# Performance work log

Hardware: AMD Instinct MI355X
Metric: run time of the kernel (lower is better)

## Reference

```python
import jax, jax.numpy as jnp
import numpy as np

N_NODES = 100000
N_EDGES = 1600000

def setup_inputs() -> dict:
    key = jax.random.key(0)
    ks = jax.random.split(key, 6)
    x = jax.random.normal(ks[0], (N_NODES, 128), dtype=jnp.float32)
    edge_index = jax.random.randint(ks[1], (2, N_EDGES), 0, N_NODES, dtype=jnp.int64)
    edge_weight = jax.random.uniform(ks[2], (N_EDGES,), dtype=jnp.float32)
    # kaiming-uniform-like init for weights, zeros for biases (as in reset_parameters)
    bound1 = float(np.sqrt(6.0 / 128))
    W1 = jax.random.uniform(ks[3], (128, 128), minval=-bound1, maxval=bound1, dtype=jnp.float32)
    b1 = jnp.zeros((128,), dtype=jnp.float32)
    W2 = jax.random.uniform(ks[4], (128, 64), minval=-bound1, maxval=bound1, dtype=jnp.float32)
    b2 = jnp.zeros((64,), dtype=jnp.float32)
    return {"x": x, "edge_index": edge_index, "edge_weight": edge_weight,
            "W1": W1, "b1": b1, "W2": W2, "b2": b2}

def _gcn_conv(x, src, dst, ew, W, b):
    support = x @ W                      # [N, F_out] dense GEMM
    msgs = ew[:, None] * support[src]    # [E, F_out] gather + scale (spmm values)
    out = jax.ops.segment_sum(msgs, dst, num_segments=N_NODES)  # scatter-add
    return out + b

def reference(x, edge_index, edge_weight, W1, b1, W2, b2):
    dst, src = edge_index[0], edge_index[1]  # adj[dst, src] = edge_weight
    h = _gcn_conv(x, src, dst, edge_weight, W1, b1)
    h = jax.nn.relu(h)
    out = _gcn_conv(h, src, dst, edge_weight, W2, b2)
    return out
```

## Files before the change

kernel.cpp:

```cpp
#include <hip/hip_runtime.h>

#define N_NODES 100000
#define N_EDGES 1600000
#define NB 391
#define PAD 16
#define SC_EPB 2048
#define SC_BLOCKS ((N_EDGES + SC_EPB - 1) / SC_EPB)
#define LDA 136
#define NTILES ((N_NODES + 127) / 128)

typedef unsigned int uint32;
typedef __attribute__((ext_vector_type(8))) short bf16x8;
typedef __attribute__((ext_vector_type(4))) float f32x4;

__device__ __forceinline__ uint32 bf16_rne(float f) {
    uint32 u = __float_as_uint(f);
    return (u + 0x7fffu + ((u >> 16) & 1u)) >> 16;
}
__device__ __forceinline__ uint32 pack_bf16x2(float lo, float hi) {
    return bf16_rne(lo) | (bf16_rne(hi) << 16);
}
__device__ __forceinline__ float bf16_lo(uint32 u) { return __uint_as_float(u << 16); }
__device__ __forceinline__ float bf16_hi(uint32 u) { return __uint_as_float(u & 0xFFFF0000u); }

__global__ __launch_bounds__(256) void conv_x(const float* __restrict__ x,
                                              uint32* __restrict__ xb) {
    const int t = blockIdx.x * 256 + threadIdx.x;
    if (t >= N_NODES * 64) return;
    const float2 v = ((const float2*)x)[t];
    xb[t] = pack_bf16x2(v.x, v.y);
}

__global__ __launch_bounds__(256) void conv_w(const float* __restrict__ W1,
                                              const float* __restrict__ W2,
                                              uint32* __restrict__ w1tb,
                                              uint32* __restrict__ w2tb) {
    const int t = blockIdx.x * 256 + threadIdx.x;
    if (t < 128 * 64) {
        const int n = t >> 6, kk = t & 63;
        w1tb[t] = pack_bf16x2(W1[(2 * kk) * 128 + n], W1[(2 * kk + 1) * 128 + n]);
    } else if (t < 128 * 64 + 64 * 64) {
        const int u = t - 128 * 64;
        const int n = u >> 6, kk = u & 63;
        w2tb[u] = pack_bf16x2(W2[(2 * kk) * 64 + n], W2[(2 * kk + 1) * 64 + n]);
    }
}

__global__ __launch_bounds__(256) void bucket_hist(const int* __restrict__ dst,
                                                   int* __restrict__ bktCnt) {
    __shared__ int h[NB];
    for (int i = threadIdx.x; i < NB; i += 256) h[i] = 0;
    __syncthreads();
    for (int e = blockIdx.x * 256 + threadIdx.x; e < N_EDGES; e += NB * 256)
        atomicAdd(&h[dst[e] >> 8], 1);
    __syncthreads();
    for (int i = threadIdx.x; i < NB; i += 256)
        if (h[i]) atomicAdd(&bktCnt[i * PAD], h[i]);
}

__global__ __launch_bounds__(512) void bucket_scan(const int* __restrict__ bktCnt,
                                                   int* __restrict__ bBase,
                                                   int* __restrict__ bCur,
                                                   int* __restrict__ offs) {
    __shared__ int s[512];
    const int t = threadIdx.x;
    int v = (t < NB) ? bktCnt[t * PAD] : 0;
    s[t] = v;
    __syncthreads();
#pragma unroll
    for (int off = 1; off < 512; off <<= 1) {
        int u = (t >= off) ? s[t - off] : 0;
        __syncthreads();
        s[t] += u;
        __syncthreads();
    }
    if (t < NB) {
        const int excl = s[t] - v;
        bBase[t] = excl;
        bCur[t * PAD] = excl;
    }
    if (t == 0) {
        bBase[NB] = N_EDGES;
        offs[N_NODES] = N_EDGES;
    }
}

__global__ __launch_bounds__(256) void bucket_scatter2(const int* __restrict__ dst,
                                                       const int* __restrict__ src,
                                                       const float* __restrict__ ew,
                                                       int* __restrict__ bCur,
                                                       int2* __restrict__ bucketed) {
    __shared__ int h[NB];
    __shared__ int cur[NB];
    const int base = blockIdx.x * SC_EPB;
    const int end  = min(base + SC_EPB, N_EDGES);

    for (int i = threadIdx.x; i < NB; i += 256) h[i] = 0;
    __syncthreads();
    for (int e = base + threadIdx.x; e < end; e += 256)
        atomicAdd(&h[dst[e] >> 8], 1);
    __syncthreads();
    for (int i = threadIdx.x; i < NB; i += 256) {
        const int c = h[i];
        cur[i] = c ? atomicAdd(&bCur[i * PAD], c) : 0;
    }
    __syncthreads();
    for (int e = base + threadIdx.x; e < end; e += 256) {
        const int d = dst[e];
        const int p = atomicAdd(&cur[d >> 8], 1);
        bucketed[p] = make_int2(src[e] | ((d & 255) << 17), __float_as_int(ew[e]));
    }
}

__global__ __launch_bounds__(256) void bucket_csr(const int2* __restrict__ bucketed,
                                                  const int* __restrict__ bBase,
                                                  int* __restrict__ offs,
                                                  int2* __restrict__ csr_ef) {
    __shared__ int sdeg[256];
    __shared__ int lcur[256];
    const int b   = blockIdx.x;
    const int t   = threadIdx.x;
    const int beg = bBase[b], end = bBase[b + 1];

    sdeg[t] = 0;
    __syncthreads();
    for (int j = beg + t; j < end; j += 256)
        atomicAdd(&sdeg[(bucketed[j].x >> 17) & 255], 1);
    __syncthreads();
    const int mydeg = sdeg[t];
#pragma unroll
    for (int off = 1; off < 256; off <<= 1) {
        int u = (t >= off) ? sdeg[t - off] : 0;
        __syncthreads();
        sdeg[t] += u;
        __syncthreads();
    }
    const int excl = sdeg[t] - mydeg;
    lcur[t] = excl;
    const int node = b * 256 + t;
    if (node < N_NODES) offs[node] = beg + excl;
    __syncthreads();

    for (int j = beg + t; j < end; j += 256) {
        const int2 v = bucketed[j];
        const int dl = (v.x >> 17) & 255;
        const int p  = beg + atomicAdd(&lcur[dl], 1);
        csr_ef[p] = make_int2(v.x & 0x1FFFF, v.y);
    }
}

template <int FEAT>
__global__ __launch_bounds__(256) void aggregate(const void* __restrict__ featv,
                                                 const int* __restrict__ offs,
                                                 const int2* __restrict__ csr_ef,
                                                 const float* __restrict__ bias,
                                                 void* __restrict__ outv) {
    const int n    = (blockIdx.x * 256 + threadIdx.x) >> 6;
    const int lane = threadIdx.x & 63;
    if (n >= N_NODES) return;
    const int beg = offs[n], end = offs[n + 1];

    if constexpr (FEAT == 128) {
        const uint32* feat = (const uint32*)featv;
        float2 acc = make_float2(0.f, 0.f);
        int j = beg;
        for (; j + 3 < end; j += 4) {
            const int2 e0 = csr_ef[j],     e1 = csr_ef[j + 1];
            const int2 e2 = csr_ef[j + 2], e3 = csr_ef[j + 3];
            const uint32 v0 = feat[(size_t)e0.x * 64 + lane];
            const uint32 v1 = feat[(size_t)e1.x * 64 + lane];
            const uint32 v2 = feat[(size_t)e2.x * 64 + lane];
            const uint32 v3 = feat[(size_t)e3.x * 64 + lane];
            const float w0 = __int_as_float(e0.y), w1 = __int_as_float(e1.y);
            const float w2 = __int_as_float(e2.y), w3 = __int_as_float(e3.y);
            acc.x += w0 * bf16_lo(v0) + w1 * bf16_lo(v1) + w2 * bf16_lo(v2) + w3 * bf16_lo(v3);
            acc.y += w0 * bf16_hi(v0) + w1 * bf16_hi(v1) + w2 * bf16_hi(v2) + w3 * bf16_hi(v3);
        }
        for (; j < end; ++j) {
            const int2 e0 = csr_ef[j];
            const uint32 v = feat[(size_t)e0.x * 64 + lane];
            const float w = __int_as_float(e0.y);
            acc.x += w * bf16_lo(v);
            acc.y += w * bf16_hi(v);
        }
        ((uint32*)outv)[(size_t)n * 64 + lane] = pack_bf16x2(acc.x, acc.y);
    } else {
        const unsigned short* feat = (const unsigned short*)featv;
        float acc = bias[lane];
        int j = beg;
        for (; j + 3 < end; j += 4) {
            const int2 e0 = csr_ef[j],     e1 = csr_ef[j + 1];
            const int2 e2 = csr_ef[j + 2], e3 = csr_ef[j + 3];
            const float f0 = __uint_as_float((uint32)feat[(size_t)e0.x * 64 + lane] << 16);
            const float f1 = __uint_as_float((uint32)feat[(size_t)e1.x * 64 + lane] << 16);
            const float f2 = __uint_as_float((uint32)feat[(size_t)e2.x * 64 + lane] << 16);
            const float f3 = __uint_as_float((uint32)feat[(size_t)e3.x * 64 + lane] << 16);
            acc += __int_as_float(e0.y) * f0 + __int_as_float(e1.y) * f1
                 + __int_as_float(e2.y) * f2 + __int_as_float(e3.y) * f3;
        }
        for (; j < end; ++j) {
            const int2 e0 = csr_ef[j];
            acc += __int_as_float(e0.y)
                 * __uint_as_float((uint32)feat[(size_t)e0.x * 64 + lane] << 16);
        }
        ((float*)outv)[(size_t)n * 64 + lane] = acc;
    }
}

__global__ __launch_bounds__(512) void gemm_fused(const uint32* __restrict__ aggPb,
                                                  const uint32* __restrict__ w1tb,
                                                  const float* __restrict__ b1,
                                                  const uint32* __restrict__ w2tb,
                                                  uint32* __restrict__ sup2b, int N) {
    __shared__ __align__(16) short As[128 * LDA];
    __shared__ __align__(16) short W1s[128 * LDA];
    __shared__ __align__(16) short W2s[64 * LDA];
    __shared__ __align__(16) short Ts[128 * LDA];

    const int tid = threadIdx.x;

    for (int i = tid; i < 128 * 16; i += 512)
        *(uint4*)&W1s[(i >> 4) * LDA + (i & 15) * 8] = ((const uint4*)w1tb)[i];
    for (int i = tid; i < 64 * 16; i += 512)
        *(uint4*)&W2s[(i >> 4) * LDA + (i & 15) * 8] = ((const uint4*)w2tb)[i];

    const int wave = tid >> 6;
    const int lane = tid & 63;
    const int m    = lane & 15;
    const int quad = lane >> 4;
    const int rowbase = (wave & 3) * 32;
    const int colbase = (wave >> 2) * 64;

    float b1r[4];
#pragma unroll
    for (int ct = 0; ct < 4; ++ct) b1r[ct] = b1[colbase + ct * 16 + m];

    for (int tile = blockIdx.x; tile < NTILES; tile += gridDim.x) {
        const int row0 = tile * 128;
        __syncthreads();

#pragma unroll
        for (int i = 0; i < 4; ++i) {
            const int idx = i * 512 + tid;
            const int row = idx >> 4, c4 = idx & 15;
            const int grow = row0 + row;
            uint4 v = make_uint4(0u, 0u, 0u, 0u);
            if (grow < N) v = ((const uint4*)aggPb)[(size_t)grow * 16 + c4];
            *(uint4*)&As[row * LDA + c4 * 8] = v;
        }
        __syncthreads();

        bf16x8 afrag[2][4];
#pragma unroll
        for (int ss = 0; ss < 2; ++ss)
#pragma unroll
            for (int ch = 0; ch < 4; ++ch)
                afrag[ss][ch] = *(const bf16x8*)&As[(rowbase + ss * 16 + m) * LDA + ch * 32 + quad * 8];

        f32x4 acc[2][4];
#pragma unroll
        for (int ss = 0; ss < 2; ++ss)
#pragma unroll
            for (int ct = 0; ct < 4; ++ct) acc[ss][ct] = (f32x4){0.f, 0.f, 0.f, 0.f};

#pragma unroll
        for (int ct = 0; ct < 4; ++ct) {
            bf16x8 bfr[4];
#pragma unroll
            for (int ch = 0; ch < 4; ++ch)
                bfr[ch] = *(const bf16x8*)&W1s[(colbase + ct * 16 + m) * LDA + ch * 32 + quad * 8];
#pragma unroll
            for (int ss = 0; ss < 2; ++ss)
#pragma unroll
                for (int ch = 0; ch < 4; ++ch)
                    acc[ss][ct] = __builtin_amdgcn_mfma_f32_16x16x32_bf16(
                        afrag[ss][ch], bfr[ch], acc[ss][ct], 0, 0, 0);
        }

#pragma unroll
        for (int ss = 0; ss < 2; ++ss)
#pragma unroll
            for (int ct = 0; ct < 4; ++ct)
#pragma unroll
                for (int r = 0; r < 4; ++r) {
                    const float v = fmaxf(acc[ss][ct][r] + b1r[ct], 0.f);
                    const int row = rowbase + ss * 16 + quad * 4 + r;
                    const int col = colbase + ct * 16 + m;
                    Ts[row * LDA + col] = (short)bf16_rne(v);
                }
        __syncthreads();

        const int rb2 = wave * 16;
        bf16x8 tfrag[4];
#pragma unroll
        for (int ch = 0; ch < 4; ++ch)
            tfrag[ch] = *(const bf16x8*)&Ts[(rb2 + m) * LDA + ch * 32 + quad * 8];

        f32x4 acc2[4];
#pragma unroll
        for (int ct = 0; ct < 4; ++ct) acc2[ct] = (f32x4){0.f, 0.f, 0.f, 0.f};
#pragma unroll
        for (int ct = 0; ct < 4; ++ct)
#pragma unroll
            for (int ch = 0; ch < 4; ++ch) {
                const bf16x8 bfr = *(const bf16x8*)&W2s[(ct * 16 + m) * LDA + ch * 32 + quad * 8];
                acc2[ct] = __builtin_amdgcn_mfma_f32_16x16x32_bf16(
                    tfrag[ch], bfr, acc2[ct], 0, 0, 0);
            }

#pragma unroll
        for (int ct = 0; ct < 4; ++ct)
#pragma unroll
            for (int r = 0; r < 4; ++r) {
                const int row = rb2 + quad * 4 + r;
                const int col = ct * 16 + m;
                As[row * LDA + col] = (short)bf16_rne(acc2[ct][r]);
            }
        __syncthreads();
#pragma unroll
        for (int i = 0; i < 2; ++i) {
            const int idx = i * 512 + tid;
            const int row = idx >> 3, c4 = idx & 7;
            if (row0 + row < N)
                ((uint4*)sup2b)[(size_t)(row0 + row) * 8 + c4] = *(uint4*)&As[row * LDA + c4 * 8];
        }
    }
}

extern "C" void kernel_launch(void* const* d_in, const int* in_sizes, int n_in,
                              void* d_out, int out_size, void* d_ws, size_t ws_size,
                              hipStream_t stream) {
    const float* x  = (const float*)d_in[0];
    const int*   ei = (const int*)d_in[1];
    const float* ew = (const float*)d_in[2];
    const float* W1 = (const float*)d_in[3];
    const float* b1 = (const float*)d_in[4];
    const float* W2 = (const float*)d_in[5];
    const float* b2 = (const float*)d_in[6];
    float* out = (float*)d_out;

    const int* dstIdx = ei;
    const int* srcIdx = ei + N_EDGES;

    uint32* xb      = (uint32*)d_ws;
    uint32* aggPb   = xb + (size_t)N_NODES * 64;
    uint32* w1tb    = aggPb + (size_t)N_NODES * 64;
    uint32* w2tb    = w1tb + 128 * 64;
    int2*   csr_ef  = (int2*)(xb + (size_t)N_NODES * 64 + (size_t)N_NODES * 128);
    int*    bktCnt  = (int*)(csr_ef + N_EDGES);
    int*    bCur    = bktCnt + NB * PAD;
    int*    bBase   = bCur + NB * PAD;
    int*    offs    = bBase + NB + 1;
    int2*   bucketed = (int2*)aggPb;
    uint32* sup2b   = xb;

    (void)hipMemsetAsync(bktCnt, 0, (size_t)NB * PAD * sizeof(int), stream);
    conv_x<<<(N_NODES * 64 + 255) / 256, 256, 0, stream>>>(x, xb);
    conv_w<<<48, 256, 0, stream>>>(W1, W2, w1tb, w2tb);

    bucket_hist<<<NB, 256, 0, stream>>>(dstIdx, bktCnt);
    bucket_scan<<<1, 512, 0, stream>>>(bktCnt, bBase, bCur, offs);
    bucket_scatter2<<<SC_BLOCKS, 256, 0, stream>>>(dstIdx, srcIdx, ew, bCur, bucketed);
    bucket_csr<<<NB, 256, 0, stream>>>(bucketed, bBase, offs, csr_ef);

    aggregate<128><<<(N_NODES * 64) / 256, 256, 0, stream>>>(xb, offs, csr_ef,
                                                             nullptr, aggPb);
    gemm_fused<<<256, 512, 0, stream>>>(aggPb, w1tb, b1, w2tb, sup2b, N_NODES);

    aggregate<64><<<(N_NODES * 64) / 256, 256, 0, stream>>>(sup2b, offs, csr_ef,
                                                            b2, out);
}
```

Baseline: 363.6 us.

## Split aggregate wavefront into edge groups with 16-byte feature loads and shuffle reduction

Each 64-lane wavefront in the aggregation kernel now splits into 4 groups of 16 lanes (128-wide features) or 8 groups of 8 lanes (64-wide features). Each group processes a different edge and loads 8 bf16 values per lane with one 16-byte load, where before every lane read one 4- or 2-byte value per edge. Partial sums are combined with xor shuffles and a single group writes the result with vector stores. This aims to keep more gathers in flight and cut the number of load instructions, at the cost of shuffle reductions and idle lanes on low-degree nodes.

```diff
diff --git a/kernel.cpp b/kernel.cpp
--- a/kernel.cpp
+++ b/kernel.cpp
@@ -159,51 +159,100 @@
     const int lane = threadIdx.x & 63;
     if (n >= N_NODES) return;
     const int beg = offs[n], end = offs[n + 1];
+    const uint4* feat = (const uint4*)featv;
+
+    float a0 = 0.f, a1 = 0.f, a2 = 0.f, a3 = 0.f;
+    float a4 = 0.f, a5 = 0.f, a6 = 0.f, a7 = 0.f;
 
     if constexpr (FEAT == 128) {
-        const uint32* feat = (const uint32*)featv;
-        float2 acc = make_float2(0.f, 0.f);
-        int j = beg;
-        for (; j + 3 < end; j += 4) {
-            const int2 e0 = csr_ef[j],     e1 = csr_ef[j + 1];
-            const int2 e2 = csr_ef[j + 2], e3 = csr_ef[j + 3];
-            const uint32 v0 = feat[(size_t)e0.x * 64 + lane];
-            const uint32 v1 = feat[(size_t)e1.x * 64 + lane];
-            const uint32 v2 = feat[(size_t)e2.x * 64 + lane];
-            const uint32 v3 = feat[(size_t)e3.x * 64 + lane];
-            const float w0 = __int_as_float(e0.y), w1 = __int_as_float(e1.y);
-            const float w2 = __int_as_float(e2.y), w3 = __int_as_float(e3.y);
-            acc.x += w0 * bf16_lo(v0) + w1 * bf16_lo(v1) + w2 * bf16_lo(v2) + w3 * bf16_lo(v3);
-            acc.y += w0 * bf16_hi(v0) + w1 * bf16_hi(v1) + w2 * bf16_hi(v2) + w3 * bf16_hi(v3);
-        }
-        for (; j < end; ++j) {
-            const int2 e0 = csr_ef[j];
-            const uint32 v = feat[(size_t)e0.x * 64 + lane];
-            const float w = __int_as_float(e0.y);
-            acc.x += w * bf16_lo(v);
-            acc.y += w * bf16_hi(v);
-        }
-        ((uint32*)outv)[(size_t)n * 64 + lane] = pack_bf16x2(acc.x, acc.y);
+        const int g  = lane >> 4;
+        const int f8 = lane & 15;
+
+        for (int j = beg + g; j < end; j += 8) {
+            {
+                const int2 e = csr_ef[j];
+                const uint4 r = feat[(unsigned)(e.x * 16 + f8)];
+                const float w = __int_as_float(e.y);
+                a0 += w * bf16_lo(r.x); a1 += w * bf16_hi(r.x);
+                a2 += w * bf16_lo(r.y); a3 += w * bf16_hi(r.y);
+                a4 += w * bf16_lo(r.z); a5 += w * bf16_hi(r.z);
+                a6 += w * bf16_lo(r.w); a7 += w * bf16_hi(r.w);
+            }
+            if (j + 4 < end) {
+                const int2 e = csr_ef[j + 4];
+                const uint4 r = feat[(unsigned)(e.x * 16 + f8)];
+                const float w = __int_as_float(e.y);
+                a0 += w * bf16_lo(r.x); a1 += w * bf16_hi(r.x);
+                a2 += w * bf16_lo(r.y); a3 += w * bf16_hi(r.y);
+                a4 += w * bf16_lo(r.z); a5 += w * bf16_hi(r.z);
+                a6 += w * bf16_lo(r.w); a7 += w * bf16_hi(r.w);
+            }
+        }
+
+        a0 += __shfl_xor(a0, 16); a1 += __shfl_xor(a1, 16);
+        a2 += __shfl_xor(a2, 16); a3 += __shfl_xor(a3, 16);
+        a4 += __shfl_xor(a4, 16); a5 += __shfl_xor(a5, 16);
+        a6 += __shfl_xor(a6, 16); a7 += __shfl_xor(a7, 16);
+        a0 += __shfl_xor(a0, 32); a1 += __shfl_xor(a1, 32);
+        a2 += __shfl_xor(a2, 32); a3 += __shfl_xor(a3, 32);
+        a4 += __shfl_xor(a4, 32); a5 += __shfl_xor(a5, 32);
+        a6 += __shfl_xor(a6, 32); a7 += __shfl_xor(a7, 32);
+
+        if (g == 0) {
+            uint4 p;
+            p.x = pack_bf16x2(a0, a1);
+            p.y = pack_bf16x2(a2, a3);
+            p.z = pack_bf16x2(a4, a5);
+            p.w = pack_bf16x2(a6, a7);
+            ((uint4*)outv)[(size_t)n * 16 + f8] = p;
+        }
     } else {
-        const unsigned short* feat = (const unsigned short*)featv;
-        float acc = bias[lane];
-        int j = beg;
-        for (; j + 3 < end; j += 4) {
-            const int2 e0 = csr_ef[j],     e1 = csr_ef[j + 1];
-            const int2 e2 = csr_ef[j + 2], e3 = csr_ef[j + 3];
-            const float f0 = __uint_as_float((uint32)feat[(size_t)e0.x * 64 + lane] << 16);
-            const float f1 = __uint_as_float((uint32)feat[(size_t)e1.x * 64 + lane] << 16);
-            const float f2 = __uint_as_float((uint32)feat[(size_t)e2.x * 64 + lane] << 16);
-            const float f3 = __uint_as_float((uint32)feat[(size_t)e3.x * 64 + lane] << 16);
-            acc += __int_as_float(e0.y) * f0 + __int_as_float(e1.y) * f1
-                 + __int_as_float(e2.y) * f2 + __int_as_float(e3.y) * f3;
-        }
-        for (; j < end; ++j) {
-            const int2 e0 = csr_ef[j];
-            acc += __int_as_float(e0.y)
-                 * __uint_as_float((uint32)feat[(size_t)e0.x * 64 + lane] << 16);
-        }
-        ((float*)outv)[(size_t)n * 64 + lane] = acc;
+        const int g  = lane >> 3;
+        const int f4 = lane & 7;
+
+        for (int j = beg + g; j < end; j += 16) {
+            {
+                const int2 e = csr_ef[j];
+                const uint4 r = feat[(unsigned)(e.x * 8 + f4)];
+                const float w = __int_as_float(e.y);
+                a0 += w * bf16_lo(r.x); a1 += w * bf16_hi(r.x);
+                a2 += w * bf16_lo(r.y); a3 += w * bf16_hi(r.y);
+                a4 += w * bf16_lo(r.z); a5 += w * bf16_hi(r.z);
+                a6 += w * bf16_lo(r.w); a7 += w * bf16_hi(r.w);
+            }
+            if (j + 8 < end) {
+                const int2 e = csr_ef[j + 8];
+                const uint4 r = feat[(unsigned)(e.x * 8 + f4)];
+                const float w = __int_as_float(e.y);
+                a0 += w * bf16_lo(r.x); a1 += w * bf16_hi(r.x);
+                a2 += w * bf16_lo(r.y); a3 += w * bf16_hi(r.y);
+                a4 += w * bf16_lo(r.z); a5 += w * bf16_hi(r.z);
+                a6 += w * bf16_lo(r.w); a7 += w * bf16_hi(r.w);
+            }
+        }
+
+        a0 += __shfl_xor(a0, 8);  a1 += __shfl_xor(a1, 8);
+        a2 += __shfl_xor(a2, 8);  a3 += __shfl_xor(a3, 8);
+        a4 += __shfl_xor(a4, 8);  a5 += __shfl_xor(a5, 8);
+        a6 += __shfl_xor(a6, 8);  a7 += __shfl_xor(a7, 8);
+        a0 += __shfl_xor(a0, 16); a1 += __shfl_xor(a1, 16);
+        a2 += __shfl_xor(a2, 16); a3 += __shfl_xor(a3, 16);
+        a4 += __shfl_xor(a4, 16); a5 += __shfl_xor(a5, 16);
+        a6 += __shfl_xor(a6, 16); a7 += __shfl_xor(a7, 16);
+        a0 += __shfl_xor(a0, 32); a1 += __shfl_xor(a1, 32);
+        a2 += __shfl_xor(a2, 32); a3 += __shfl_xor(a3, 32);
+        a4 += __shfl_xor(a4, 32); a5 += __shfl_xor(a5, 32);
+        a6 += __shfl_xor(a6, 32); a7 += __shfl_xor(a7, 32);
+
+        if (g == 0) {
+            const float4* b4 = (const float4*)bias;
+            const float4 bA = b4[f4 * 2];
+            const float4 bB = b4[f4 * 2 + 1];
+            float4 o0 = make_float4(a0 + bA.x, a1 + bA.y, a2 + bA.z, a3 + bA.w);
+            float4 o1 = make_float4(a4 + bB.x, a5 + bB.y, a6 + bB.z, a7 + bB.w);
+            ((float4*)outv)[(size_t)n * 16 + f4 * 2]     = o0;
+            ((float4*)outv)[(size_t)n * 16 + f4 * 2 + 1] = o1;
+        }
     }
 }
 
```

New measurement: 337.2 us. 7.3% less time.

## Split aggregation into feature slices with edge-parallel lanes and shuffle reduction

Applied to the files above, without the earlier changes.

Replaces the one-wavefront-per-node aggregation with a sliced scheme. Each node's feature columns are split across NSLICE blocks, and within a wavefront the lanes are grouped so that several edges are gathered in parallel. Partial sums are then combined with xor shuffles. The aim is more memory-level parallelism per node and fewer serial dependent edge loads, at the cost of reading csr_ef NSLICE times, shuffle overhead, and smaller gathered segments per row.

```diff
diff --git a/kernel.cpp b/kernel.cpp
--- a/kernel.cpp
+++ b/kernel.cpp
@@ -8,6 +8,7 @@
 #define SC_BLOCKS ((N_EDGES + SC_EPB - 1) / SC_EPB)
 #define LDA 136
 #define NTILES ((N_NODES + 127) / 128)
+#define NSLICE 4
 
 typedef unsigned int uint32;
 typedef __attribute__((ext_vector_type(8))) short bf16x8;
@@ -150,60 +151,54 @@
 }
 
 template <int FEAT>
-__global__ __launch_bounds__(256) void aggregate(const void* __restrict__ featv,
-                                                 const int* __restrict__ offs,
-                                                 const int2* __restrict__ csr_ef,
-                                                 const float* __restrict__ bias,
-                                                 void* __restrict__ outv) {
-    const int n    = (blockIdx.x * 256 + threadIdx.x) >> 6;
+__global__ __launch_bounds__(256) void aggregate_sl(const uint32* __restrict__ feat,
+                                                    const int* __restrict__ offs,
+                                                    const int2* __restrict__ csr_ef,
+                                                    const float* __restrict__ bias,
+                                                    void* __restrict__ outv) {
+    constexpr int ROWU   = FEAT / 2;
+    constexpr int SLICEU = ROWU / NSLICE;
+    constexpr int G      = 64 / SLICEU;
+    constexpr int U      = (FEAT == 128) ? 4 : 2;
+
+    const int slice = blockIdx.x & (NSLICE - 1);
+    const int n     = (blockIdx.x >> 2) * 4 + (threadIdx.x >> 6);
+    if (n >= N_NODES) return;
     const int lane = threadIdx.x & 63;
-    if (n >= N_NODES) return;
+    const int f    = lane & (SLICEU - 1);
+    const int g    = lane / SLICEU;
+    const int col  = slice * SLICEU + f;
+
     const int beg = offs[n], end = offs[n + 1];
-
-    if constexpr (FEAT == 128) {
-        const uint32* feat = (const uint32*)featv;
-        float2 acc = make_float2(0.f, 0.f);
-        int j = beg;
-        for (; j + 3 < end; j += 4) {
-            const int2 e0 = csr_ef[j],     e1 = csr_ef[j + 1];
-            const int2 e2 = csr_ef[j + 2], e3 = csr_ef[j + 3];
-            const uint32 v0 = feat[(size_t)e0.x * 64 + lane];
-            const uint32 v1 = feat[(size_t)e1.x * 64 + lane];
-            const uint32 v2 = feat[(size_t)e2.x * 64 + lane];
-            const uint32 v3 = feat[(size_t)e3.x * 64 + lane];
-            const float w0 = __int_as_float(e0.y), w1 = __int_as_float(e1.y);
-            const float w2 = __int_as_float(e2.y), w3 = __int_as_float(e3.y);
-            acc.x += w0 * bf16_lo(v0) + w1 * bf16_lo(v1) + w2 * bf16_lo(v2) + w3 * bf16_lo(v3);
-            acc.y += w0 * bf16_hi(v0) + w1 * bf16_hi(v1) + w2 * bf16_hi(v2) + w3 * bf16_hi(v3);
-        }
-        for (; j < end; ++j) {
-            const int2 e0 = csr_ef[j];
-            const uint32 v = feat[(size_t)e0.x * 64 + lane];
-            const float w = __int_as_float(e0.y);
-            acc.x += w * bf16_lo(v);
-            acc.y += w * bf16_hi(v);
-        }
-        ((uint32*)outv)[(size_t)n * 64 + lane] = pack_bf16x2(acc.x, acc.y);
-    } else {
-        const unsigned short* feat = (const unsigned short*)featv;
-        float acc = bias[lane];
-        int j = beg;
-        for (; j + 3 < end; j += 4) {
-            const int2 e0 = csr_ef[j],     e1 = csr_ef[j + 1];
-            const int2 e2 = csr_ef[j + 2], e3 = csr_ef[j + 3];
-            const float f0 = __uint_as_float((uint32)feat[(size_t)e0.x * 64 + lane] << 16);
-            const float f1 = __uint_as_float((uint32)feat[(size_t)e1.x * 64 + lane] << 16);
-            const float f2 = __uint_as_float((uint32)feat[(size_t)e2.x * 64 + lane] << 16);
-            const float f3 = __uint_as_float((uint32)feat[(size_t)e3.x * 64 + lane] << 16);
-            acc += __int_as_float(e0.y) * f0 + __int_as_float(e1.y) * f1
-                 + __int_as_float(e2.y) * f2 + __int_as_float(e3.y) * f3;
-        }
-        for (; j < end; ++j) {
-            const int2 e0 = csr_ef[j];
-            acc += __int_as_float(e0.y)
-                 * __uint_as_float((uint32)feat[(size_t)e0.x * 64 + lane] << 16);
-        }
-        ((float*)outv)[(size_t)n * 64 + lane] = acc;
+    float a0 = 0.f, a1 = 0.f;
+
+    for (int j = beg + g; j < end; j += U * G) {
+#pragma unroll
+        for (int u = 0; u < U; ++u) {
+            const int jj = j + u * G;
+            if (u == 0 || jj < end) {
+                const int2 e = csr_ef[jj];
+                const uint32 r = feat[(unsigned)(e.x * ROWU + col)];
+                const float w = __int_as_float(e.y);
+                a0 += w * bf16_lo(r);
+                a1 += w * bf16_hi(r);
+            }
+        }
+    }
+
+#pragma unroll
+    for (int d = SLICEU; d < 64; d <<= 1) {
+        a0 += __shfl_xor(a0, d);
+        a1 += __shfl_xor(a1, d);
+    }
+
+    if (g == 0) {
+        if constexpr (FEAT == 128) {
+            ((uint32*)outv)[(size_t)n * 64 + col] = pack_bf16x2(a0, a1);
+        } else {
+            const float2 b = ((const float2*)bias)[col];
+            ((float2*)outv)[(size_t)n * 32 + col] = make_float2(a0 + b.x, a1 + b.y);
+        }
     }
 }
 
@@ -363,10 +358,11 @@
     bucket_scatter2<<<SC_BLOCKS, 256, 0, stream>>>(dstIdx, srcIdx, ew, bCur, bucketed);
     bucket_csr<<<NB, 256, 0, stream>>>(bucketed, bBase, offs, csr_ef);
 
-    aggregate<128><<<(N_NODES * 64) / 256, 256, 0, stream>>>(xb, offs, csr_ef,
-                                                             nullptr, aggPb);
+    const int aggBlocks = NSLICE * ((N_NODES + 3) / 4);
+    aggregate_sl<128><<<aggBlocks, 256, 0, stream>>>(xb, offs, csr_ef,
+                                                     nullptr, aggPb);
     gemm_fused<<<256, 512, 0, stream>>>(aggPb, w1tb, b1, w2tb, sup2b, N_NODES);
 
-    aggregate<64><<<(N_NODES * 64) / 256, 256, 0, stream>>>(sup2b, offs, csr_ef,
-                                                            b2, out);
-}
+    aggregate_sl<64><<<aggBlocks, 256, 0, stream>>>(sup2b, offs, csr_ef,
+                                                    b2, out);
+}
```

After: 578.2 us. +59.0%, slower.
